# Optimization experiments

Hardware: AMD Instinct MI355X
Metric: run time of the kernel (lower is better)

Reference implementation:

```python
import jax, jax.numpy as jnp
import numpy as np

SHAPE = (32, 512, 512)  # (D, H, W) dense voxel grid
N_ACTIVE = 150000


def setup_inputs() -> dict:
    key = jax.random.key(0)
    k_f, k_w1, k_w2 = jax.random.split(key, 3)
    D, H, W = SHAPE
    # unique active voxel coordinates (collision-free dense-grid hash)
    rng = np.random.default_rng(0)
    lin = rng.permutation(D * H * W)[:N_ACTIVE]
    z = lin // (H * W)
    y = (lin // W) % H
    x = lin % W
    coors = np.stack([np.zeros(N_ACTIVE, np.int32), z.astype(np.int32),
                      y.astype(np.int32), x.astype(np.int32)], axis=1)
    features = jax.random.normal(k_f, (N_ACTIVE, 3), dtype=jnp.float32)
    # per-offset GEMM weights: [K^3, Cin, Cout]
    w1 = jax.random.normal(k_w1, (27, 3, 128), dtype=jnp.float32) * 0.2
    w2 = jax.random.normal(k_w2, (27, 128, 128), dtype=jnp.float32) * 0.05
    return {"features": features, "coors": jnp.asarray(coors), "w1": w1,
            "w2": w2, "batch_size": 1}


def _build_grid(coors):
    D, H, W = SHAPE
    n = coors.shape[0]
    grid = jnp.full((D, H, W), -1, dtype=jnp.int32)
    return grid.at[coors[:, 1], coors[:, 2], coors[:, 3]].set(
        jnp.arange(n, dtype=jnp.int32))


def _subm_conv3d(feat, coors, grid, w):
    """Submanifold 3x3x3 conv: gather active neighbors per offset, GEMM, accumulate.
    feat: [N, Cin]; w: [27, Cin, Cout]; output defined only on active sites -> [N, Cout]."""
    D, H, W = SHAPE
    n = feat.shape[0]
    out = jnp.zeros((n, w.shape[-1]), dtype=feat.dtype)
    k = 0
    for dz in (-1, 0, 1):
        for dy in (-1, 0, 1):
            for dx in (-1, 0, 1):
                nz = coors[:, 1] + dz
                ny = coors[:, 2] + dy
                nx = coors[:, 3] + dx
                inb = ((nz >= 0) & (nz < D) & (ny >= 0) & (ny < H)
                       & (nx >= 0) & (nx < W))
                nidx = grid[jnp.clip(nz, 0, D - 1), jnp.clip(ny, 0, H - 1),
                            jnp.clip(nx, 0, W - 1)]
                valid = inb & (nidx >= 0)
                g = jnp.where(valid[:, None],
                              feat[jnp.clip(nidx, 0, n - 1)], 0.0)  # [N, Cin]
                out = out + g @ w[k]
                k += 1
    return out


def reference(features, coors, w1, w2, batch_size):
    # SparseConvTensor: features [N,3], coors [N,4] (batch,z,y,x), batch_size=1
    grid = _build_grid(coors)
    h = _subm_conv3d(features, coors, grid, w1)   # SubMConv3d(3, 128, 3)
    out = _subm_conv3d(h, coors, grid, w2)        # SubMConv3d(128, 128, 3), shared indice_key
    return out
```

## Files before the change

### kernel.cpp

```cpp
#include <hip/hip_runtime.h>
#include <stdint.h>

#define GD 32
#define GH 512
#define GW 512
#define GDHW (GD * GH * GW)
#define KOFF 27
#define CAP 4096
#define CNTS 32
#define NW2 (KOFF * 128 * 128)

typedef __attribute__((ext_vector_type(8))) short short8;
typedef __attribute__((ext_vector_type(4))) float f32x4;

__device__ __forceinline__ unsigned short f32_to_bf16(float x) {
    unsigned int u = __float_as_uint(x);
    unsigned int r = (u + 0x7FFFu + ((u >> 16) & 1u)) >> 16;
    return (unsigned short)r;
}

__global__ __launch_bounds__(256) void setup_kernel(
    const int* __restrict__ coors, int* __restrict__ grid,
    unsigned int* __restrict__ bitgrid,
    const float* __restrict__ w2, unsigned short* __restrict__ w2t,
    int* __restrict__ cnts, int n, int nbsc) {
    const int bid = blockIdx.x, t = threadIdx.x;
    if (bid == 0) {
        for (int q = t; q < 26 * CNTS + 32; q += 256) cnts[q] = 0;
    }
    if (bid < nbsc) {
        int i = bid * 256 + t;
        if (i < n) {
            int z = coors[i * 4 + 1];
            int y = coors[i * 4 + 2];
            int x = coors[i * 4 + 3];
            int cell = (z * GH + y) * GW + x;
            grid[cell] = i;
            atomicOr(&bitgrid[cell >> 5], 1u << (cell & 31));
        }
    } else {
        int g = (bid - nbsc) * 256 + t;
        if (g < NW2) {
            int k = g >> 14;
            int c = (g >> 7) & 127;
            int q = g & 127;
            w2t[g] = f32_to_bf16(w2[(k * 128 + q) * 128 + c]);
        }
    }
}

__global__ __launch_bounds__(256) void nbr_kernel(
    const int* __restrict__ coors, const int* __restrict__ grid,
    const unsigned int* __restrict__ bitgrid,
    int* __restrict__ vcnt, int* __restrict__ nbrc,
    int* __restrict__ pairs, int* __restrict__ npos,
    int* __restrict__ cnts, int* __restrict__ rn,
    int* __restrict__ rlist, int n) {
    __shared__ int wcnt[4][26];
    __shared__ int kbase[26];

    const int i = blockIdx.x * 256 + threadIdx.x;
    const int t = threadIdx.x, wave = t >> 6, lane = t & 63;
    const bool live = (i < n);
    const unsigned long long lmask = (1ull << lane) - 1;

    int z = 0, y = 0, x = 0;
    if (live) {
        z = coors[i * 4 + 1];
        y = coors[i * 4 + 2];
        x = coors[i * 4 + 3];
    }

    int j[27];
#pragma unroll
    for (int k = 0; k < 27; ++k) {
        if (k == 13) { j[k] = live ? i : -1; continue; }
        int dz = k / 9 - 1, dy = (k / 3) % 3 - 1, dx = k % 3 - 1;
        int nz = z + dz, ny = y + dy, nx = x + dx;
        int cz = min(max(nz, 0), GD - 1);
        int cy = min(max(ny, 0), GH - 1);
        int cx = min(max(nx, 0), GW - 1);
        int cell = (cz * GH + cy) * GW + cx;
        bool ok = live && nz >= 0 && nz < GD && ny >= 0 && ny < GH &&
                  nx >= 0 && nx < GW;
        unsigned int word = bitgrid[cell >> 5];
        bool occ = ok && ((word >> (cell & 31)) & 1u);
        j[k] = occ ? grid[cell] : -1;
    }

    int c = 0;
    if (live) {
#pragma unroll
        for (int k = 0; k < 27; ++k) {
            if (k == 13) continue;
            if (j[k] >= 0) { nbrc[i * 27 + c] = (k << 20) | j[k]; ++c; }
        }
        vcnt[i] = c;
    }

    {
        unsigned long long mr = __ballot(live && c > 0);
        int rbase = 0;
        if (lane == 0 && mr) rbase = atomicAdd(rn, __popcll(mr));
        rbase = __shfl(rbase, 0);
        if (live && c > 0) rlist[rbase + __popcll(mr & lmask)] = i;
    }

#pragma unroll
    for (int kk = 0; kk < 26; ++kk) {
        const int k = kk + (kk >= 13);
        unsigned long long m = __ballot(live && (j[k] >= 0));
        if (lane == 0) wcnt[wave][kk] = __popcll(m);
    }
    __syncthreads();
    if (t < 26) {
        int tot = wcnt[0][t] + wcnt[1][t] + wcnt[2][t] + wcnt[3][t];
        kbase[t] = (tot > 0) ? atomicAdd(&cnts[t * CNTS], tot) : 0;
    }
    __syncthreads();
    int slot = 0;
#pragma unroll
    for (int kk = 0; kk < 26; ++kk) {
        const int k = kk + (kk >= 13);
        const bool valid = live && (j[k] >= 0);
        unsigned long long m = __ballot(valid);
        if (valid) {
            int off = 0;
#pragma unroll
            for (int w = 0; w < 4; ++w)
                if (w < wave) off += wcnt[w][kk];
            int pos = kbase[kk] + off + __popcll(m & lmask);
            if (pos < CAP) {
                pairs[kk * CAP + pos] = j[k];
                npos[i * 27 + slot] = kk * CAP + pos;
            } else {
                npos[i * 27 + slot] = -1;
            }
            ++slot;
        }
    }
}

__global__ __launch_bounds__(256) void conv1_kernel(
    const float* __restrict__ feat, const float* __restrict__ w1,
    const int* __restrict__ vcnt, const int* __restrict__ nbrc,
    unsigned short* __restrict__ hout, int n) {
    const int wave = threadIdx.x >> 6, lane = threadIdx.x & 63;
    const int i = blockIdx.x * 4 + wave;
    if (i >= n) return;
    const int c2 = lane * 2;

    const int cnt = vcnt[i];
    float f0 = feat[i * 3 + 0];
    float f1 = feat[i * 3 + 1];
    float f2 = feat[i * 3 + 2];

    const float* wc = w1 + 13 * 384 + c2;
    float2 w0 = *(const float2*)(wc);
    float2 wv1 = *(const float2*)(wc + 128);
    float2 w2_ = *(const float2*)(wc + 256);
    float a0 = f0 * w0.x + f1 * wv1.x + f2 * w2_.x;
    float a1 = f0 * w0.y + f1 * wv1.y + f2 * w2_.y;

    for (int s = 0; s < cnt; ++s) {
        int e = nbrc[i * 27 + s];
        int k = e >> 20, jj = e & 0xFFFFF;
        float g0 = feat[jj * 3 + 0];
        float g1 = feat[jj * 3 + 1];
        float g2 = feat[jj * 3 + 2];
        const float* wk = w1 + k * 384 + c2;
        float2 u0 = *(const float2*)(wk);
        float2 u1 = *(const float2*)(wk + 128);
        float2 u2 = *(const float2*)(wk + 256);
        a0 += g0 * u0.x + g1 * u1.x + g2 * u2.x;
        a1 += g0 * u0.y + g1 * u1.y + g2 * u2.y;
    }

    unsigned int packed = (unsigned int)f32_to_bf16(a0) |
                          ((unsigned int)f32_to_bf16(a1) << 16);
    *(unsigned int*)(hout + (size_t)i * 128 + c2) = packed;
}

__global__ __launch_bounds__(256, 2) void conv2a_kernel(
    const unsigned short* __restrict__ h,
    const unsigned short* __restrict__ w2t,
    float* __restrict__ out, int n) {
    const int t = threadIdx.x;
    const int wave = t >> 6, lane = t & 63;
    const int lane16 = lane & 15, quad = lane >> 4;
    const int wm = wave >> 1, wn = wave & 1;
    const int row0 = blockIdx.x * 128;

    short8 a[4][4];
#pragma unroll
    for (int ms = 0; ms < 4; ++ms) {
        int r = row0 + wm * 64 + ms * 16 + lane16;
        r = min(r, n - 1);
        const unsigned short* hp = h + (size_t)r * 128 + quad * 8;
#pragma unroll
        for (int ks = 0; ks < 4; ++ks)
            a[ms][ks] = *(const short8*)(hp + ks * 32);
    }

    short8 b[4][4];
    const unsigned short* wbase = w2t + 13 * 16384 + quad * 8;
#pragma unroll
    for (int ns = 0; ns < 4; ++ns) {
        int c = wn * 64 + ns * 16 + lane16;
        const unsigned short* wp = wbase + c * 128;
#pragma unroll
        for (int ks = 0; ks < 4; ++ks)
            b[ns][ks] = *(const short8*)(wp + ks * 32);
    }

    f32x4 acc[4][4];
#pragma unroll
    for (int p = 0; p < 4; ++p)
#pragma unroll
        for (int q = 0; q < 4; ++q) acc[p][q] = (f32x4){0.f, 0.f, 0.f, 0.f};

#pragma unroll
    for (int ks = 0; ks < 4; ++ks)
#pragma unroll
        for (int ns = 0; ns < 4; ++ns)
#pragma unroll
            for (int ms = 0; ms < 4; ++ms)
                acc[ms][ns] = __builtin_amdgcn_mfma_f32_16x16x32_bf16(
                    a[ms][ks], b[ns][ks], acc[ms][ns], 0, 0, 0);

#pragma unroll
    for (int ms = 0; ms < 4; ++ms) {
#pragma unroll
        for (int r = 0; r < 4; ++r) {
            int i = row0 + wm * 64 + ms * 16 + quad * 4 + r;
            if (i < n) {
#pragma unroll
                for (int ns = 0; ns < 4; ++ns) {
                    int col = wn * 64 + ns * 16 + lane16;
                    out[(size_t)i * 128 + col] = acc[ms][ns][r];
                }
            }
        }
    }
}

__global__ __launch_bounds__(256, 2) void conv2b_kernel(
    const unsigned short* __restrict__ h,
    const unsigned short* __restrict__ w2t,
    const int* __restrict__ pairs, const int* __restrict__ cnts,
    unsigned short* __restrict__ corr) {
    const int kb = blockIdx.x >> 5;
    const int tile = blockIdx.x & 31;
    const int cnt = min(cnts[kb * CNTS], CAP);
    const int base = tile * 128;
    if (base >= cnt) return;
    const int m = min(128, cnt - base);
    const int k = kb + (kb >= 13);
    const int* pk = pairs + kb * CAP + base;

    const int t = threadIdx.x;
    const int wave = t >> 6, lane = t & 63;
    const int lane16 = lane & 15, quad = lane >> 4;
    const int wm = wave >> 1, wn = wave & 1;

    short8 a[4][4];
#pragma unroll
    for (int ms = 0; ms < 4; ++ms) {
        int r = wm * 64 + ms * 16 + lane16;
        bool v = (r < m);
        int j = v ? pk[r] : 0;
        const unsigned short* hp = h + (size_t)j * 128 + quad * 8;
#pragma unroll
        for (int ks = 0; ks < 4; ++ks)
            a[ms][ks] = v ? *(const short8*)(hp + ks * 32)
                          : (short8){0, 0, 0, 0, 0, 0, 0, 0};
    }

    short8 b[4][4];
    const unsigned short* wbase = w2t + (size_t)k * 16384 + quad * 8;
#pragma unroll
    for (int ns = 0; ns < 4; ++ns) {
        int c = wn * 64 + ns * 16 + lane16;
        const unsigned short* wp = wbase + c * 128;
#pragma unroll
        for (int ks = 0; ks < 4; ++ks)
            b[ns][ks] = *(const short8*)(wp + ks * 32);
    }

    f32x4 acc[4][4];
#pragma unroll
    for (int p = 0; p < 4; ++p)
#pragma unroll
        for (int q = 0; q < 4; ++q) acc[p][q] = (f32x4){0.f, 0.f, 0.f, 0.f};

#pragma unroll
    for (int ks = 0; ks < 4; ++ks)
#pragma unroll
        for (int ns = 0; ns < 4; ++ns)
#pragma unroll
            for (int ms = 0; ms < 4; ++ms)
                acc[ms][ns] = __builtin_amdgcn_mfma_f32_16x16x32_bf16(
                    a[ms][ks], b[ns][ks], acc[ms][ns], 0, 0, 0);

#pragma unroll
    for (int ms = 0; ms < 4; ++ms) {
#pragma unroll
        for (int r = 0; r < 4; ++r) {
            int row = wm * 64 + ms * 16 + quad * 4 + r;
            if (row < m) {
                unsigned short* cr =
                    corr + (size_t)(kb * CAP + base + row) * 128;
#pragma unroll
                for (int ns = 0; ns < 4; ++ns) {
                    int col = wn * 64 + ns * 16 + lane16;
                    cr[col] = f32_to_bf16(acc[ms][ns][r]);
                }
            }
        }
    }
}

__global__ __launch_bounds__(256) void fixup_kernel(
    const unsigned short* __restrict__ corr, const int* __restrict__ vcnt,
    const int* __restrict__ npos, const int* __restrict__ rlist,
    const int* __restrict__ rn, float* __restrict__ out) {
    const int widx = blockIdx.x * 4 + (threadIdx.x >> 6);
    const int lane = threadIdx.x & 63;
    if (widx >= rn[0]) return;
    const int i = rlist[widx];
    const int cnt = vcnt[i];
    const int* np = npos + i * 27;

    float a0 = 0.f, a1 = 0.f;
    for (int s = 0; s < cnt; ++s) {
        int p = np[s];
        if (p >= 0) {
            unsigned int u =
                *(const unsigned int*)(corr + (size_t)p * 128 + lane * 2);
            a0 += __uint_as_float(u << 16);
            a1 += __uint_as_float(u & 0xFFFF0000u);
        }
    }
    float2* op = (float2*)(out + (size_t)i * 128) + lane;
    float2 cur = *op;
    cur.x += a0;
    cur.y += a1;
    *op = cur;
}

extern "C" void kernel_launch(void* const* d_in, const int* in_sizes, int n_in,
                              void* d_out, int out_size, void* d_ws,
                              size_t ws_size, hipStream_t stream) {
    const float* feat = (const float*)d_in[0];
    const int* coors = (const int*)d_in[1];
    const float* w1 = (const float*)d_in[2];
    const float* w2 = (const float*)d_in[3];
    float* out = (float*)d_out;

    const int n = in_sizes[0] / 3;

    uint8_t* ws = (uint8_t*)d_ws;
    size_t off = 0;
    int* grid = (int*)(ws + off); off += (size_t)GDHW * 4;
    unsigned int* bitgrid = (unsigned int*)(ws + off);
    off += (size_t)(GDHW / 8);
    int* vcnt = (int*)(ws + off); off += (size_t)n * 4;
    int* nbrc = (int*)(ws + off); off += (size_t)n * 27 * 4;
    int* npos = (int*)(ws + off); off += (size_t)n * 27 * 4;
    int* rlist = (int*)(ws + off); off += (size_t)n * 4;
    off = (off + 255) & ~(size_t)255;
    unsigned short* hbuf = (unsigned short*)(ws + off);
    off += (size_t)n * 128 * 2;
    off = (off + 255) & ~(size_t)255;
    unsigned short* w2t = (unsigned short*)(ws + off);
    off += (size_t)KOFF * 128 * 128 * 2;
    off = (off + 255) & ~(size_t)255;
    int* pairs = (int*)(ws + off);
    off += (size_t)26 * CAP * 4;
    off = (off + 255) & ~(size_t)255;
    int* cnts = (int*)(ws + off); off += (26 * CNTS + 32) * 4;
    int* rn = cnts + 26 * CNTS;
    off = (off + 255) & ~(size_t)255;
    unsigned short* corr = (unsigned short*)(ws + off);
    off += (size_t)26 * CAP * 128 * 2;

    hipMemsetAsync(bitgrid, 0x00, (size_t)(GDHW / 8), stream);

    const int nbsc = (n + 255) / 256;
    const int nbw2 = (NW2 + 255) / 256;
    setup_kernel<<<nbsc + nbw2, 256, 0, stream>>>(coors, grid, bitgrid, w2,
                                                  w2t, cnts, n, nbsc);
    nbr_kernel<<<nbsc, 256, 0, stream>>>(coors, grid, bitgrid, vcnt, nbrc,
                                         pairs, npos, cnts, rn, rlist, n);
    conv1_kernel<<<(n + 3) / 4, 256, 0, stream>>>(feat, w1, vcnt, nbrc, hbuf, n);
    conv2b_kernel<<<26 * 32, 256, 0, stream>>>(hbuf, w2t, pairs, cnts, corr);
    conv2a_kernel<<<(n + 127) / 128, 256, 0, stream>>>(hbuf, w2t, out, n);
    fixup_kernel<<<(n + 3) / 4, 256, 0, stream>>>(corr, vcnt, npos, rlist, rn,
                                                  out);
}
```

Baseline: 259.0 us.

## Replace atomic pair compaction with deterministic block-count scan pipeline

The neighbor-build kernel is split into three kernels: one that records per-wave ballot masks and per-block counts per offset, a 26-block prefix scan over block counts, and one that writes pairs and positions using the scanned bases. This removes the per-block global atomics on the offset counters and the atomic row list. The fixup kernel now iterates over all voxels and exits early when a voxel has no neighbors. The cost is two extra kernel launches, extra mask and count traffic, and a serial per-offset scan over roughly 590 blocks.

```diff
diff --git a/kernel.cpp b/kernel.cpp
--- a/kernel.cpp
+++ b/kernel.cpp
@@ -23,11 +23,8 @@
     const int* __restrict__ coors, int* __restrict__ grid,
     unsigned int* __restrict__ bitgrid,
     const float* __restrict__ w2, unsigned short* __restrict__ w2t,
-    int* __restrict__ cnts, int n, int nbsc) {
+    int n, int nbsc) {
     const int bid = blockIdx.x, t = threadIdx.x;
-    if (bid == 0) {
-        for (int q = t; q < 26 * CNTS + 32; q += 256) cnts[q] = 0;
-    }
     if (bid < nbsc) {
         int i = bid * 256 + t;
         if (i < n) {
@@ -49,20 +46,18 @@
     }
 }
 
-__global__ __launch_bounds__(256) void nbr_kernel(
+__global__ __launch_bounds__(256) void nbr1_kernel(
     const int* __restrict__ coors, const int* __restrict__ grid,
     const unsigned int* __restrict__ bitgrid,
     int* __restrict__ vcnt, int* __restrict__ nbrc,
-    int* __restrict__ pairs, int* __restrict__ npos,
-    int* __restrict__ cnts, int* __restrict__ rn,
-    int* __restrict__ rlist, int n) {
+    unsigned long long* __restrict__ wmask, int* __restrict__ bcnt,
+    int n, int nb) {
     __shared__ int wcnt[4][26];
-    __shared__ int kbase[26];
-
-    const int i = blockIdx.x * 256 + threadIdx.x;
+
+    const int bid = blockIdx.x;
+    const int i = bid * 256 + threadIdx.x;
     const int t = threadIdx.x, wave = t >> 6, lane = t & 63;
     const bool live = (i < n);
-    const unsigned long long lmask = (1ull << lane) - 1;
 
     int z = 0, y = 0, x = 0;
     if (live) {
@@ -88,8 +83,8 @@
         j[k] = occ ? grid[cell] : -1;
     }
 
-    int c = 0;
     if (live) {
+        int c = 0;
 #pragma unroll
         for (int k = 0; k < 27; ++k) {
             if (k == 13) continue;
@@ -98,45 +93,85 @@
         vcnt[i] = c;
     }
 
-    {
-        unsigned long long mr = __ballot(live && c > 0);
-        int rbase = 0;
-        if (lane == 0 && mr) rbase = atomicAdd(rn, __popcll(mr));
-        rbase = __shfl(rbase, 0);
-        if (live && c > 0) rlist[rbase + __popcll(mr & lmask)] = i;
-    }
-
 #pragma unroll
     for (int kk = 0; kk < 26; ++kk) {
         const int k = kk + (kk >= 13);
         unsigned long long m = __ballot(live && (j[k] >= 0));
-        if (lane == 0) wcnt[wave][kk] = __popcll(m);
+        if (lane == 0) {
+            wmask[((size_t)bid * 4 + wave) * 26 + kk] = m;
+            wcnt[wave][kk] = __popcll(m);
+        }
     }
     __syncthreads();
+    if (t < 26)
+        bcnt[t * nb + bid] = wcnt[0][t] + wcnt[1][t] + wcnt[2][t] + wcnt[3][t];
+}
+
+__global__ __launch_bounds__(256) void scan_kernel(
+    const int* __restrict__ bcnt, int* __restrict__ bbase,
+    int* __restrict__ cnts, int nb) {
+    const int k = blockIdx.x;
+    const int t = threadIdx.x;
+    __shared__ int s[256];
+    int run = 0;
+    for (int base = 0; base < nb; base += 256) {
+        int idx = base + t;
+        int v = (idx < nb) ? bcnt[k * nb + idx] : 0;
+        s[t] = v;
+        __syncthreads();
+        for (int off = 1; off < 256; off <<= 1) {
+            int u = (t >= off) ? s[t - off] : 0;
+            __syncthreads();
+            s[t] += u;
+            __syncthreads();
+        }
+        int incl = s[t];
+        int total = s[255];
+        if (idx < nb) bbase[k * nb + idx] = run + incl - v;
+        run += total;
+        __syncthreads();
+    }
+    if (t == 0) cnts[k * CNTS] = run;
+}
+
+__global__ __launch_bounds__(256) void nbr2_kernel(
+    const int* __restrict__ vcnt, const int* __restrict__ nbrc,
+    const unsigned long long* __restrict__ wmask,
+    const int* __restrict__ bbase,
+    int* __restrict__ pairs, int* __restrict__ npos, int n, int nb) {
+    __shared__ unsigned long long lmsk[4][26];
+    __shared__ int woff[4][26];
+    __shared__ int bb[26];
+
+    const int bid = blockIdx.x;
+    const int t = threadIdx.x, wave = t >> 6, lane = t & 63;
     if (t < 26) {
-        int tot = wcnt[0][t] + wcnt[1][t] + wcnt[2][t] + wcnt[3][t];
-        kbase[t] = (tot > 0) ? atomicAdd(&cnts[t * CNTS], tot) : 0;
+        unsigned long long m0 = wmask[((size_t)bid * 4 + 0) * 26 + t];
+        unsigned long long m1 = wmask[((size_t)bid * 4 + 1) * 26 + t];
+        unsigned long long m2 = wmask[((size_t)bid * 4 + 2) * 26 + t];
+        unsigned long long m3 = wmask[((size_t)bid * 4 + 3) * 26 + t];
+        lmsk[0][t] = m0; lmsk[1][t] = m1; lmsk[2][t] = m2; lmsk[3][t] = m3;
+        int p0 = __popcll(m0), p1 = __popcll(m1), p2 = __popcll(m2);
+        woff[0][t] = 0; woff[1][t] = p0; woff[2][t] = p0 + p1;
+        woff[3][t] = p0 + p1 + p2;
+        bb[t] = bbase[t * nb + bid];
     }
     __syncthreads();
-    int slot = 0;
-#pragma unroll
-    for (int kk = 0; kk < 26; ++kk) {
-        const int k = kk + (kk >= 13);
-        const bool valid = live && (j[k] >= 0);
-        unsigned long long m = __ballot(valid);
-        if (valid) {
-            int off = 0;
-#pragma unroll
-            for (int w = 0; w < 4; ++w)
-                if (w < wave) off += wcnt[w][kk];
-            int pos = kbase[kk] + off + __popcll(m & lmask);
-            if (pos < CAP) {
-                pairs[kk * CAP + pos] = j[k];
-                npos[i * 27 + slot] = kk * CAP + pos;
-            } else {
-                npos[i * 27 + slot] = -1;
-            }
-            ++slot;
+
+    const int i = bid * 256 + t;
+    if (i >= n) return;
+    const unsigned long long lmask = (1ull << lane) - 1;
+    const int cnt = vcnt[i];
+    for (int s = 0; s < cnt; ++s) {
+        int e = nbrc[i * 27 + s];
+        int k = e >> 20, j = e & 0xFFFFF;
+        int kk = k - (k > 13);
+        int pos = bb[kk] + woff[wave][kk] + __popcll(lmsk[wave][kk] & lmask);
+        if (pos < CAP) {
+            pairs[kk * CAP + pos] = j;
+            npos[i * 27 + s] = kk * CAP + pos;
+        } else {
+            npos[i * 27 + s] = -1;
         }
     }
 }
@@ -322,13 +357,12 @@
 
 __global__ __launch_bounds__(256) void fixup_kernel(
     const unsigned short* __restrict__ corr, const int* __restrict__ vcnt,
-    const int* __restrict__ npos, const int* __restrict__ rlist,
-    const int* __restrict__ rn, float* __restrict__ out) {
-    const int widx = blockIdx.x * 4 + (threadIdx.x >> 6);
+    const int* __restrict__ npos, float* __restrict__ out, int n) {
+    const int i = blockIdx.x * 4 + (threadIdx.x >> 6);
     const int lane = threadIdx.x & 63;
-    if (widx >= rn[0]) return;
-    const int i = rlist[widx];
+    if (i >= n) return;
     const int cnt = vcnt[i];
+    if (cnt == 0) return;
     const int* np = npos + i * 27;
 
     float a0 = 0.f, a1 = 0.f;
@@ -358,6 +392,7 @@
     float* out = (float*)d_out;
 
     const int n = in_sizes[0] / 3;
+    const int nb = (n + 255) / 256;
 
     uint8_t* ws = (uint8_t*)d_ws;
     size_t off = 0;
@@ -367,7 +402,11 @@
     int* vcnt = (int*)(ws + off); off += (size_t)n * 4;
     int* nbrc = (int*)(ws + off); off += (size_t)n * 27 * 4;
     int* npos = (int*)(ws + off); off += (size_t)n * 27 * 4;
-    int* rlist = (int*)(ws + off); off += (size_t)n * 4;
+    off = (off + 255) & ~(size_t)255;
+    unsigned long long* wmask = (unsigned long long*)(ws + off);
+    off += (size_t)nb * 4 * 26 * 8;
+    int* bcnt = (int*)(ws + off); off += (size_t)26 * nb * 4;
+    int* bbase = (int*)(ws + off); off += (size_t)26 * nb * 4;
     off = (off + 255) & ~(size_t)255;
     unsigned short* hbuf = (unsigned short*)(ws + off);
     off += (size_t)n * 128 * 2;
@@ -378,23 +417,23 @@
     int* pairs = (int*)(ws + off);
     off += (size_t)26 * CAP * 4;
     off = (off + 255) & ~(size_t)255;
-    int* cnts = (int*)(ws + off); off += (26 * CNTS + 32) * 4;
-    int* rn = cnts + 26 * CNTS;
+    int* cnts = (int*)(ws + off); off += 26 * CNTS * 4;
     off = (off + 255) & ~(size_t)255;
     unsigned short* corr = (unsigned short*)(ws + off);
     off += (size_t)26 * CAP * 128 * 2;
 
     hipMemsetAsync(bitgrid, 0x00, (size_t)(GDHW / 8), stream);
 
-    const int nbsc = (n + 255) / 256;
     const int nbw2 = (NW2 + 255) / 256;
-    setup_kernel<<<nbsc + nbw2, 256, 0, stream>>>(coors, grid, bitgrid, w2,
-                                                  w2t, cnts, n, nbsc);
-    nbr_kernel<<<nbsc, 256, 0, stream>>>(coors, grid, bitgrid, vcnt, nbrc,
-                                         pairs, npos, cnts, rn, rlist, n);
+    setup_kernel<<<nb + nbw2, 256, 0, stream>>>(coors, grid, bitgrid, w2, w2t,
+                                                n, nb);
+    nbr1_kernel<<<nb, 256, 0, stream>>>(coors, grid, bitgrid, vcnt, nbrc,
+                                        wmask, bcnt, n, nb);
+    scan_kernel<<<26, 256, 0, stream>>>(bcnt, bbase, cnts, nb);
+    nbr2_kernel<<<nb, 256, 0, stream>>>(vcnt, nbrc, wmask, bbase, pairs, npos,
+                                        n, nb);
     conv1_kernel<<<(n + 3) / 4, 256, 0, stream>>>(feat, w1, vcnt, nbrc, hbuf, n);
     conv2b_kernel<<<26 * 32, 256, 0, stream>>>(hbuf, w2t, pairs, cnts, corr);
     conv2a_kernel<<<(n + 127) / 128, 256, 0, stream>>>(hbuf, w2t, out, n);
-    fixup_kernel<<<(n + 3) / 4, 256, 0, stream>>>(corr, vcnt, npos, rlist, rn,
-                                                  out);
-}
+    fixup_kernel<<<(n + 3) / 4, 256, 0, stream>>>(corr, vcnt, npos, out, n);
+}
```

Result: faster. 246.5 us (-4.8%).
